# Performance work log

Hardware: AMD Instinct MI355X
Metric: run time of the kernel (lower is better)

The kernel has to match this reference:

```python
import jax, jax.numpy as jnp
import numpy as np

EPS = 1e-7  # keras K.epsilon()
ROUTINGS = 3


def squash(v, axis=-1):
    s = jnp.sum(v * v, axis=axis, keepdims=True)
    scale = s / (1.0 + s) / jnp.sqrt(s + EPS)
    return scale * v


def setup_inputs() -> dict:
    key = jax.random.key(0)
    k1, k2 = jax.random.split(key)
    B, I, K = 256, 2048, 8   # batch, input_num_capsule, input_dim_capsule
    J, D = 10, 16            # num_capsule, dim_capsule
    inputs = jax.random.normal(k1, (B, I, K), dtype=jnp.float32)
    W = jax.random.normal(k2, (J, I, D, K), dtype=jnp.float32) * 0.05
    return {"inputs": inputs, "W": W}


def reference(inputs, W):
    # inputs: [B, I, K]; W: [J, I, D, K]
    # inputs_hat[b,j,i,d] = W[j,i] @ inputs[b,i]  -> [B, J, I, D]
    u_hat = jnp.einsum('jidk,bik->bjid', W, inputs)
    B, J, I, _ = u_hat.shape
    b = jnp.zeros((B, J, 1, I), dtype=u_hat.dtype)
    outputs = None
    for r in range(ROUTINGS):
        c = jax.nn.softmax(b, axis=1)                       # softmax over output capsules
        s = jnp.einsum('bjqi,bjid->bjqd', c, u_hat)          # [B, J, 1, D]
        outputs = squash(s, axis=-1)
        if r < ROUTINGS - 1:
            b = b + jnp.einsum('bjqd,bjid->bjqi', outputs, u_hat)
    return jnp.squeeze(outputs, axis=2)                      # [B, J, D]
```

## Files before the change

kernel.cpp:

```cpp
#include <hip/hip_runtime.h>
#include <math.h>


#define BB 256
#define II 2048
#define KK 8
#define JJ 10
#define DD 16
#define NCH 128
#define NBLK 512

typedef __attribute__((ext_vector_type(4))) float f32x4;
typedef __attribute__((ext_vector_type(8))) short short8;

__device__ __forceinline__ short f2bf(float f) {
    union { float f; unsigned u; } v; v.f = f;
    unsigned r = v.u + 0x7FFFu + ((v.u >> 16) & 1u);
    return (short)(r >> 16);
}

__global__ __launch_bounds__(256) void prep_kernel(const float* __restrict__ x,
                                                   const float* __restrict__ W,
                                                   short* __restrict__ xTb,
                                                   short* __restrict__ Wb,
                                                   int* __restrict__ cnt) {
    __shared__ float4 tile[8 * 66];
    const int t = threadIdx.x;
    if (blockIdx.x == 0 && t < 16) cnt[t] = 0;

    for (int r = blockIdx.x * 256 + t; r < JJ * II * DD; r += NBLK * 256) {
        const float4* src = (const float4*)(W + (size_t)r * 8);
        const float4 a = src[0], b = src[1];
        short8 o;
        o[0] = f2bf(a.x); o[1] = f2bf(a.y); o[2] = f2bf(a.z); o[3] = f2bf(a.w);
        o[4] = f2bf(b.x); o[5] = f2bf(b.y); o[6] = f2bf(b.z); o[7] = f2bf(b.w);
        *(short8*)(Wb + (size_t)r * 8) = o;
    }

    for (int tl = blockIdx.x; tl < 2048; tl += NBLK) {
        const int i0 = (tl & 255) * 8, b0 = (tl >> 8) * 32;
        __syncthreads();
        {
            const int lb = t >> 3, li = t & 7;
            const float4* src = (const float4*)(x + ((b0 + lb) * II + (i0 + li)) * KK);
            tile[li * 66 + lb * 2 + 0] = src[0];
            tile[li * 66 + lb * 2 + 1] = src[1];
        }
        __syncthreads();
        {
            const int ri = t >> 5, rb = t & 31;
            const float4 p0 = tile[ri * 66 + rb * 2 + 0];
            const float4 p1 = tile[ri * 66 + rb * 2 + 1];
            short8 o;
            o[0] = f2bf(p0.x); o[1] = f2bf(p0.y); o[2] = f2bf(p0.z); o[3] = f2bf(p0.w);
            o[4] = f2bf(p1.x); o[5] = f2bf(p1.y); o[6] = f2bf(p1.z); o[7] = f2bf(p1.w);
            *(short8*)(xTb + ((size_t)(i0 + ri) * BB + (b0 + rb)) * KK) = o;
        }
    }
}

__device__ __forceinline__ void gbar(int* cnt, int phase) {
    __syncthreads();
    if (threadIdx.x == 0) {
        __threadfence();
        __hip_atomic_fetch_add(&cnt[phase], 1, __ATOMIC_RELEASE, __HIP_MEMORY_SCOPE_AGENT);
        while (__hip_atomic_load(&cnt[phase], __ATOMIC_ACQUIRE, __HIP_MEMORY_SCOPE_AGENT) < NBLK)
            __builtin_amdgcn_s_sleep(1);
    }
    __syncthreads();
}

__device__ __forceinline__ void seg_src_dst(int s, int i0, int b0,
                                            const short* __restrict__ xTb,
                                            const short* __restrict__ Wb,
                                            const short** src, int* dst) {
    if (s < 20) {
        const int j = s >> 1, h = s & 1;
        *src = Wb + ((size_t)(j * II + i0) * DD) * KK + h * 512;
        *dst = j * 1024 + h * 512;
    } else {
        const int il = s - 20;
        *src = xTb + ((size_t)(i0 + il) * BB + b0) * KK;
        *dst = 10240 + il * 512;
    }
}

template <int USE_C>
__device__ __forceinline__ void round_body(short (*L)[14336],
    const short* __restrict__ xTb, const short* __restrict__ Wb,
    const float* __restrict__ vT, float* __restrict__ p, int chunk, int bgroup)
{
    const int t = threadIdx.x;
    const int lane = t & 63, wv = t >> 6;
    const int col = lane & 15, q = lane >> 4;
    const int b0 = bgroup * 64;
    const int bl = wv * 16 + col;
    const int i0 = chunk * 16;

    short8 r0[7], r1[7];
#pragma unroll
    for (int n = 0; n < 7; ++n) {
        const int s = wv + n * 4;
        const short* src; int dst;
        seg_src_dst(s, i0, b0, xTb, Wb, &src, &dst);
        r0[n] = *(const short8*)(src + lane * 8);
        seg_src_dst(s, i0 + 8, b0, xTb, Wb, &src, &dst);
        r1[n] = *(const short8*)(src + lane * 8);
    }
#pragma unroll
    for (int n = 0; n < 7; ++n) {
        const int s = wv + n * 4;
        const short* src; int dst;
        seg_src_dst(s, i0, b0, xTb, Wb, &src, &dst);
        *(short8*)(&L[0][dst + lane * 8]) = r0[n];
    }
    __syncthreads();

    f32x4 sfrag[JJ];
#pragma unroll
    for (int j = 0; j < JJ; ++j) sfrag[j] = (f32x4){0.f, 0.f, 0.f, 0.f};

    float vfrag[JJ][4];
    if (USE_C) {
#pragma unroll
        for (int j = 0; j < JJ; ++j)
#pragma unroll
            for (int r = 0; r < 4; ++r)
                vfrag[j][r] = vT[(j * DD + q * 4 + r) * BB + b0 + bl];
    }

#pragma unroll
    for (int sc = 0; sc < 2; ++sc) {
        const short* Lb = L[sc];
        if (USE_C) {
            for (int il = 0; il < 8; ++il) {
                const short8 z = (short8){0, 0, 0, 0, 0, 0, 0, 0};
                short8 Bf = z;
                if (q == 0) Bf = *(const short8*)(&Lb[10240 + il * 512 + bl * 8]);
                f32x4 U[JJ];
                float Lg[JJ];
#pragma unroll
                for (int j = 0; j < JJ; ++j) {
                    short8 Aj = z;
                    if (q == 0) Aj = *(const short8*)(&Lb[j * 1024 + il * 128 + col * 8]);
                    U[j] = __builtin_amdgcn_mfma_f32_16x16x32_bf16(
                        Aj, Bf, (f32x4){0.f, 0.f, 0.f, 0.f}, 0, 0, 0);
                    Lg[j] = vfrag[j][0] * U[j][0] + vfrag[j][1] * U[j][1]
                          + vfrag[j][2] * U[j][2] + vfrag[j][3] * U[j][3];
                }
#pragma unroll
                for (int j = 0; j < JJ; ++j) {
                    Lg[j] += __shfl_xor(Lg[j], 16, 64);
                    Lg[j] += __shfl_xor(Lg[j], 32, 64);
                }
                float sum = 0.f;
#pragma unroll
                for (int j = 0; j < JJ; ++j) { Lg[j] = __expf(Lg[j]); sum += Lg[j]; }
                const float inv = __builtin_amdgcn_rcpf(sum);
#pragma unroll
                for (int j = 0; j < JJ; ++j) {
                    const float c = Lg[j] * inv;
#pragma unroll
                    for (int r = 0; r < 4; ++r) sfrag[j][r] += c * U[j][r];
                }
            }
        } else {
#pragma unroll
            for (int g = 0; g < 2; ++g) {
                const int il = g * 4 + q;
                const short8 Bf = *(const short8*)(&Lb[10240 + il * 512 + bl * 8]);
#pragma unroll
                for (int j = 0; j < JJ; ++j) {
                    const short8 Aj = *(const short8*)(&Lb[j * 1024 + il * 128 + col * 8]);
                    sfrag[j] = __builtin_amdgcn_mfma_f32_16x16x32_bf16(Aj, Bf, sfrag[j], 0, 0, 0);
                }
            }
        }
        if (sc == 0) {
#pragma unroll
            for (int n = 0; n < 7; ++n) {
                const int s = wv + n * 4;
                const short* src; int dst;
                seg_src_dst(s, i0 + 8, b0, xTb, Wb, &src, &dst);
                *(short8*)(&L[1][dst + lane * 8]) = r1[n];
            }
            __syncthreads();
        }
    }

    float* pp = p + ((size_t)(bgroup * 4 + wv) * NCH + chunk) * (JJ * 256);
#pragma unroll
    for (int j = 0; j < JJ; ++j)
        *(f32x4*)(pp + (j * 64 + lane) * 4) = sfrag[j];
}

template <int MODE>
__device__ __forceinline__ void rs_body(float* red, float* cf,
    const float* __restrict__ p, float* __restrict__ vT, float* __restrict__ out,
    float scale, int j, int bt)
{
    const int t = threadIdx.x;
    const int d = t >> 4, bc = t & 15;
    const int lane = (d >> 2) * 16 + bc, r = d & 3;

    const float* pp = p + (size_t)bt * NCH * (JJ * 256) + j * 256 + lane * 4 + r;
    float sum = 0.f;
#pragma unroll 8
    for (int ch = 0; ch < NCH; ++ch) sum += pp[(size_t)ch * (JJ * 256)];
    const float s = sum * scale;

    red[t] = s;
    __syncthreads();
    if (t < 16) {
        float ss = 0.f;
#pragma unroll
        for (int dd = 0; dd < DD; ++dd) {
            const float v = red[dd * 16 + t];
            ss += v * v;
        }
        cf[t] = ss / (1.f + ss) / sqrtf(ss + 1e-7f);
    }
    __syncthreads();
    const float v = cf[bc] * s;
    if (MODE == 0) vT[(j * DD + d) * BB + bt * 16 + bc] = v;
    if (MODE == 1) vT[(j * DD + d) * BB + bt * 16 + bc] += v;
    if (MODE == 2) out[((bt * 16 + bc) * JJ + j) * DD + d] = v;
}

__global__ __launch_bounds__(256, 2) void caps_kernel(
    const short* __restrict__ xTb, const short* __restrict__ Wb,
    float* __restrict__ vT, float* __restrict__ p, float* __restrict__ out,
    int* __restrict__ cnt)
{
    __shared__ short Ls[2][14336];
    float* red = (float*)&Ls[0][0];
    float* cf  = red + 256;
    const int bid = blockIdx.x;
    const int chunk = bid & (NCH - 1), bgroup = bid >> 7;
    const int rj = bid >> 4, rbt = bid & 15;

    round_body<0>(Ls, xTb, Wb, vT, p, chunk, bgroup);
    gbar(cnt, 0);
    if (bid < JJ * 16) rs_body<0>(red, cf, p, vT, out, 0.1f, rj, rbt);
    gbar(cnt, 1);
    round_body<1>(Ls, xTb, Wb, vT, p, chunk, bgroup);
    gbar(cnt, 2);
    if (bid < JJ * 16) rs_body<1>(red, cf, p, vT, out, 1.0f, rj, rbt);
    gbar(cnt, 3);
    round_body<1>(Ls, xTb, Wb, vT, p, chunk, bgroup);
    gbar(cnt, 4);
    if (bid < JJ * 16) rs_body<2>(red, cf, p, vT, out, 1.0f, rj, rbt);
}

template <int USE_C>
__global__ __launch_bounds__(256) void round_mfma_k(const short* __restrict__ xTb,
                                                    const short* __restrict__ Wb,
                                                    const float* __restrict__ vT,
                                                    float* __restrict__ p) {
    __shared__ short Ls[2][14336];
    round_body<USE_C>(Ls, xTb, Wb, vT, p, blockIdx.x, blockIdx.y);
}

template <int MODE>
__global__ __launch_bounds__(256) void rs_k(const float* __restrict__ p,
                                            float* __restrict__ vT,
                                            float* __restrict__ out, float scale) {
    __shared__ float red[256 + 16];
    rs_body<MODE>(red, red + 256, p, vT, out, scale, blockIdx.x, blockIdx.y);
}

extern "C" void kernel_launch(void* const* d_in, const int* in_sizes, int n_in,
                              void* d_out, int out_size, void* d_ws, size_t ws_size,
                              hipStream_t stream) {
    const float* x = (const float*)d_in[0];
    const float* W = (const float*)d_in[1];
    float* out = (float*)d_out;

    int*   cnt = (int*)d_ws;
    float* vT  = (float*)d_ws + 64;
    float* p   = vT + BB * JJ * DD;
    short* xTb = (short*)(p + (size_t)16 * NCH * 2560);
    short* Wb  = xTb + (size_t)II * BB * KK;

    int occ = 0;
    hipError_t oe = hipOccupancyMaxActiveBlocksPerMultiprocessor(&occ, caps_kernel, 256, 0);

    prep_kernel<<<NBLK, 256, 0, stream>>>(x, W, xTb, Wb, cnt);

    if (oe == hipSuccess && occ >= 2) {
        caps_kernel<<<NBLK, 256, 0, stream>>>(xTb, Wb, vT, p, out, cnt);
    } else {
        dim3 rg(NCH, 4);
        dim3 sg(JJ, 16);
        round_mfma_k<0><<<rg, 256, 0, stream>>>(xTb, Wb, vT, p);
        rs_k<0><<<sg, 256, 0, stream>>>(p, vT, out, 0.1f);
        round_mfma_k<1><<<rg, 256, 0, stream>>>(xTb, Wb, vT, p);
        rs_k<1><<<sg, 256, 0, stream>>>(p, vT, out, 1.0f);
        round_mfma_k<1><<<rg, 256, 0, stream>>>(xTb, Wb, vT, p);
        rs_k<2><<<sg, 256, 0, stream>>>(p, vT, out, 1.0f);
    }
}
```

Baseline: 163.3 us.

## Spread chunk reduction across all blocks and pair routing MFMA iterations

The reduce-and-squash phase previously ran on only 160 of the 512 blocks, each summing 128 chunk partials serially. It now runs on all 512 blocks, each handling 5 (batch, capsule) pairs, with the chunk sum split over 16 thread groups and combined through LDS and shuffles. Separately, the routing MFMA loop is unrolled by two so independent MFMAs and softmax work can overlap and hide latency. The cost is higher register pressure in the unrolled loop, which may hurt the two-blocks-per-CU occupancy the persistent kernel relies on.

```diff
diff --git a/kernel.cpp b/kernel.cpp
--- a/kernel.cpp
+++ b/kernel.cpp
@@ -133,35 +133,52 @@
     for (int sc = 0; sc < 2; ++sc) {
         const short* Lb = L[sc];
         if (USE_C) {
-            for (int il = 0; il < 8; ++il) {
+            for (int il = 0; il < 8; il += 2) {
                 const short8 z = (short8){0, 0, 0, 0, 0, 0, 0, 0};
-                short8 Bf = z;
-                if (q == 0) Bf = *(const short8*)(&Lb[10240 + il * 512 + bl * 8]);
-                f32x4 U[JJ];
-                float Lg[JJ];
-#pragma unroll
-                for (int j = 0; j < JJ; ++j) {
-                    short8 Aj = z;
-                    if (q == 0) Aj = *(const short8*)(&Lb[j * 1024 + il * 128 + col * 8]);
-                    U[j] = __builtin_amdgcn_mfma_f32_16x16x32_bf16(
-                        Aj, Bf, (f32x4){0.f, 0.f, 0.f, 0.f}, 0, 0, 0);
-                    Lg[j] = vfrag[j][0] * U[j][0] + vfrag[j][1] * U[j][1]
-                          + vfrag[j][2] * U[j][2] + vfrag[j][3] * U[j][3];
-                }
-#pragma unroll
-                for (int j = 0; j < JJ; ++j) {
-                    Lg[j] += __shfl_xor(Lg[j], 16, 64);
-                    Lg[j] += __shfl_xor(Lg[j], 32, 64);
-                }
-                float sum = 0.f;
-#pragma unroll
-                for (int j = 0; j < JJ; ++j) { Lg[j] = __expf(Lg[j]); sum += Lg[j]; }
-                const float inv = __builtin_amdgcn_rcpf(sum);
-#pragma unroll
-                for (int j = 0; j < JJ; ++j) {
-                    const float c = Lg[j] * inv;
-#pragma unroll
-                    for (int r = 0; r < 4; ++r) sfrag[j][r] += c * U[j][r];
+                short8 Bf0 = z, Bf1 = z;
+                if (q == 0) {
+                    Bf0 = *(const short8*)(&Lb[10240 + il * 512 + bl * 8]);
+                    Bf1 = *(const short8*)(&Lb[10240 + (il + 1) * 512 + bl * 8]);
+                }
+                f32x4 U0[JJ], U1[JJ];
+                float Lg0[JJ], Lg1[JJ];
+#pragma unroll
+                for (int j = 0; j < JJ; ++j) {
+                    short8 A0 = z, A1 = z;
+                    if (q == 0) {
+                        A0 = *(const short8*)(&Lb[j * 1024 + il * 128 + col * 8]);
+                        A1 = *(const short8*)(&Lb[j * 1024 + (il + 1) * 128 + col * 8]);
+                    }
+                    U0[j] = __builtin_amdgcn_mfma_f32_16x16x32_bf16(
+                        A0, Bf0, (f32x4){0.f, 0.f, 0.f, 0.f}, 0, 0, 0);
+                    U1[j] = __builtin_amdgcn_mfma_f32_16x16x32_bf16(
+                        A1, Bf1, (f32x4){0.f, 0.f, 0.f, 0.f}, 0, 0, 0);
+                    Lg0[j] = vfrag[j][0] * U0[j][0] + vfrag[j][1] * U0[j][1]
+                           + vfrag[j][2] * U0[j][2] + vfrag[j][3] * U0[j][3];
+                    Lg1[j] = vfrag[j][0] * U1[j][0] + vfrag[j][1] * U1[j][1]
+                           + vfrag[j][2] * U1[j][2] + vfrag[j][3] * U1[j][3];
+                }
+#pragma unroll
+                for (int j = 0; j < JJ; ++j) {
+                    Lg0[j] += __shfl_xor(Lg0[j], 16, 64);
+                    Lg1[j] += __shfl_xor(Lg1[j], 16, 64);
+                    Lg0[j] += __shfl_xor(Lg0[j], 32, 64);
+                    Lg1[j] += __shfl_xor(Lg1[j], 32, 64);
+                }
+                float sum0 = 0.f, sum1 = 0.f;
+#pragma unroll
+                for (int j = 0; j < JJ; ++j) {
+                    Lg0[j] = __expf(Lg0[j]); sum0 += Lg0[j];
+                    Lg1[j] = __expf(Lg1[j]); sum1 += Lg1[j];
+                }
+                const float inv0 = __builtin_amdgcn_rcpf(sum0);
+                const float inv1 = __builtin_amdgcn_rcpf(sum1);
+#pragma unroll
+                for (int j = 0; j < JJ; ++j) {
+                    const float c0 = Lg0[j] * inv0, c1 = Lg1[j] * inv1;
+#pragma unroll
+                    for (int r = 0; r < 4; ++r)
+                        sfrag[j][r] += c0 * U0[j][r] + c1 * U1[j][r];
                 }
             }
         } else {
@@ -194,37 +211,46 @@
         *(f32x4*)(pp + (j * 64 + lane) * 4) = sfrag[j];
 }
 
-template <int MODE>
-__device__ __forceinline__ void rs_body(float* red, float* cf,
+__device__ __forceinline__ void rs_all(float* lds,
     const float* __restrict__ p, float* __restrict__ vT, float* __restrict__ out,
-    float scale, int j, int bt)
+    float scale, int mode, int bid)
 {
     const int t = threadIdx.x;
-    const int d = t >> 4, bc = t & 15;
-    const int lane = (d >> 2) * 16 + bc, r = d & 3;
-
-    const float* pp = p + (size_t)bt * NCH * (JJ * 256) + j * 256 + lane * 4 + r;
-    float sum = 0.f;
-#pragma unroll 8
-    for (int ch = 0; ch < NCH; ++ch) sum += pp[(size_t)ch * (JJ * 256)];
-    const float s = sum * scale;
-
-    red[t] = s;
+    const int d = t & 15, g = t >> 4;
+#pragma unroll
+    for (int m = 0; m < 5; ++m) {
+        const int pid = bid * 5 + m;
+        const int b = pid / JJ, j = pid % JJ;
+        const int bt = b >> 4, bc = b & 15;
+        const float* pp = p + (size_t)bt * NCH * 2560 + j * 256
+                        + (d >> 2) * 64 + bc * 4 + (d & 3);
+        float s = 0.f;
+#pragma unroll
+        for (int sit = 0; sit < 8; ++sit) s += pp[(size_t)(g + sit * 16) * 2560];
+        lds[m * 256 + t] = s;
+    }
     __syncthreads();
     if (t < 16) {
-        float ss = 0.f;
-#pragma unroll
-        for (int dd = 0; dd < DD; ++dd) {
-            const float v = red[dd * 16 + t];
-            ss += v * v;
-        }
-        cf[t] = ss / (1.f + ss) / sqrtf(ss + 1e-7f);
-    }
-    __syncthreads();
-    const float v = cf[bc] * s;
-    if (MODE == 0) vT[(j * DD + d) * BB + bt * 16 + bc] = v;
-    if (MODE == 1) vT[(j * DD + d) * BB + bt * 16 + bc] += v;
-    if (MODE == 2) out[((bt * 16 + bc) * JJ + j) * DD + d] = v;
+#pragma unroll
+        for (int m = 0; m < 5; ++m) {
+            const int pid = bid * 5 + m;
+            const int b = pid / JJ, j = pid % JJ;
+            float s = 0.f;
+#pragma unroll
+            for (int g2 = 0; g2 < 16; ++g2) s += lds[m * 256 + g2 * 16 + t];
+            s *= scale;
+            float ss = s * s;
+            ss += __shfl_xor(ss, 1, 64);
+            ss += __shfl_xor(ss, 2, 64);
+            ss += __shfl_xor(ss, 4, 64);
+            ss += __shfl_xor(ss, 8, 64);
+            const float coef = ss / (1.f + ss) / sqrtf(ss + 1e-7f);
+            const float v = coef * s;
+            if (mode == 0)      vT[(j * DD + t) * BB + b] = v;
+            else if (mode == 1) vT[(j * DD + t) * BB + b] += v;
+            else                out[(b * JJ + j) * DD + t] = v;
+        }
+    }
 }
 
 __global__ __launch_bounds__(256, 2) void caps_kernel(
@@ -233,23 +259,21 @@
     int* __restrict__ cnt)
 {
     __shared__ short Ls[2][14336];
-    float* red = (float*)&Ls[0][0];
-    float* cf  = red + 256;
+    float* lds = (float*)&Ls[0][0];
     const int bid = blockIdx.x;
     const int chunk = bid & (NCH - 1), bgroup = bid >> 7;
-    const int rj = bid >> 4, rbt = bid & 15;
 
     round_body<0>(Ls, xTb, Wb, vT, p, chunk, bgroup);
     gbar(cnt, 0);
-    if (bid < JJ * 16) rs_body<0>(red, cf, p, vT, out, 0.1f, rj, rbt);
+    rs_all(lds, p, vT, out, 0.1f, 0, bid);
     gbar(cnt, 1);
     round_body<1>(Ls, xTb, Wb, vT, p, chunk, bgroup);
     gbar(cnt, 2);
-    if (bid < JJ * 16) rs_body<1>(red, cf, p, vT, out, 1.0f, rj, rbt);
+    rs_all(lds, p, vT, out, 1.0f, 1, bid);
     gbar(cnt, 3);
     round_body<1>(Ls, xTb, Wb, vT, p, chunk, bgroup);
     gbar(cnt, 4);
-    if (bid < JJ * 16) rs_body<2>(red, cf, p, vT, out, 1.0f, rj, rbt);
+    rs_all(lds, p, vT, out, 1.0f, 2, bid);
 }
 
 template <int USE_C>
@@ -261,12 +285,12 @@
     round_body<USE_C>(Ls, xTb, Wb, vT, p, blockIdx.x, blockIdx.y);
 }
 
-template <int MODE>
 __global__ __launch_bounds__(256) void rs_k(const float* __restrict__ p,
                                             float* __restrict__ vT,
-                                            float* __restrict__ out, float scale) {
-    __shared__ float red[256 + 16];
-    rs_body<MODE>(red, red + 256, p, vT, out, scale, blockIdx.x, blockIdx.y);
+                                            float* __restrict__ out,
+                                            float scale, int mode) {
+    __shared__ float lds[5 * 256];
+    rs_all(lds, p, vT, out, scale, mode, blockIdx.x);
 }
 
 extern "C" void kernel_launch(void* const* d_in, const int* in_sizes, int n_in,
@@ -291,12 +315,11 @@
         caps_kernel<<<NBLK, 256, 0, stream>>>(xTb, Wb, vT, p, out, cnt);
     } else {
         dim3 rg(NCH, 4);
-        dim3 sg(JJ, 16);
         round_mfma_k<0><<<rg, 256, 0, stream>>>(xTb, Wb, vT, p);
-        rs_k<0><<<sg, 256, 0, stream>>>(p, vT, out, 0.1f);
+        rs_k<<<NBLK, 256, 0, stream>>>(p, vT, out, 0.1f, 0);
         round_mfma_k<1><<<rg, 256, 0, stream>>>(xTb, Wb, vT, p);
-        rs_k<1><<<sg, 256, 0, stream>>>(p, vT, out, 1.0f);
+        rs_k<<<NBLK, 256, 0, stream>>>(p, vT, out, 1.0f, 1);
         round_mfma_k<1><<<rg, 256, 0, stream>>>(xTb, Wb, vT, p);
-        rs_k<2><<<sg, 256, 0, stream>>>(p, vT, out, 1.0f);
-    }
-}
+        rs_k<<<NBLK, 256, 0, stream>>>(p, vT, out, 1.0f, 2);
+    }
+}
```

Result: slower. 487.8 us (+198.8%).
